# Kernel optimization log

Hardware: AMD Instinct MI355X
Metric: run time of the kernel (lower is better)

## Reference

```python
import jax, jax.numpy as jnp
import numpy as np

T = 2048           # tokens (single prefill sequence)
HIDDEN = 2048
H = 16             # num heads
D_NOPE = 128
D_ROPE = 64
D_V = 128
KV_LORA = 512
EPS = 1e-6
ROPE_THETA = 10000.0


def setup_inputs() -> dict:
    key = jax.random.key(0)
    ks = jax.random.split(key, 7)
    s = 0.02
    return {
        "positions": jnp.arange(T, dtype=jnp.int64) if jax.config.jax_enable_x64 else jnp.arange(T, dtype=jnp.int32),
        "hidden_states": jax.random.normal(ks[0], (T, HIDDEN), dtype=jnp.float32),
        "w_q": jax.random.normal(ks[1], (HIDDEN, H * (D_NOPE + D_ROPE)), dtype=jnp.float32) * s,
        "w_kv_a": jax.random.normal(ks[2], (HIDDEN, KV_LORA + D_ROPE), dtype=jnp.float32) * s,
        "kv_a_ln_w": jax.random.uniform(ks[3], (KV_LORA,), dtype=jnp.float32, minval=0.5, maxval=1.5),
        "w_kv_b": jax.random.normal(ks[4], (KV_LORA, H * (D_NOPE + D_V)), dtype=jnp.float32) * s,
        "w_o": jax.random.normal(ks[5], (H * D_V, HIDDEN), dtype=jnp.float32) * s,
    }


def _rms_norm(x, w):
    var = jnp.mean(jnp.square(x), axis=-1, keepdims=True)
    return x * jax.lax.rsqrt(var + EPS) * w


def _rope_nonneox(x, positions):
    # x: [..., D_ROPE], GPT-J (interleaved) style rotation
    inv_freq = 1.0 / (ROPE_THETA ** (jnp.arange(0, D_ROPE, 2, dtype=jnp.float32) / D_ROPE))
    freqs = positions.astype(jnp.float32)[:, None] * inv_freq  # [T, D_ROPE//2]
    cos, sin = jnp.cos(freqs), jnp.sin(freqs)
    # broadcast over head dim if present
    while cos.ndim < x.ndim:
        cos, sin = cos[:, None], sin[:, None]
    x1, x2 = x[..., 0::2], x[..., 1::2]
    o1 = x1 * cos - x2 * sin
    o2 = x2 * cos + x1 * sin
    return jnp.stack([o1, o2], axis=-1).reshape(x.shape)


def reference(positions, hidden_states, w_q, w_kv_a, kv_a_ln_w, w_kv_b, w_o):
    scaling = (D_NOPE + D_ROPE) ** -0.5
    # q projection (q_lora_rank is None branch)
    q = (hidden_states @ w_q).reshape(T, H, D_NOPE + D_ROPE)
    q_nope, q_pe = q[..., :D_NOPE], q[..., D_NOPE:]
    # compressed KV latent
    latent = hidden_states @ w_kv_a                 # [T, KV_LORA + D_ROPE]
    kv_a = _rms_norm(latent[:, :KV_LORA], kv_a_ln_w)
    k_pe = latent[:, KV_LORA:]                      # [T, D_ROPE], shared across heads
    # decompress to per-head k_nope and v (kv_b_proj)
    kv = (kv_a @ w_kv_b).reshape(T, H, D_NOPE + D_V)
    k_nope, v = kv[..., :D_NOPE], kv[..., D_NOPE:]
    # non-neox RoPE
    q_pe = _rope_nonneox(q_pe, positions)
    k_pe = _rope_nonneox(k_pe, positions)           # [T, D_ROPE]
    # concat rope parts (k_pe broadcast over heads)
    q_full = jnp.concatenate([q_nope, q_pe], axis=-1)                         # [T,H,192]
    k_full = jnp.concatenate([k_nope, jnp.broadcast_to(k_pe[:, None, :], (T, H, D_ROPE))], axis=-1)
    # causal MHA
    scores = jnp.einsum("qhd,khd->hqk", q_full, k_full) * scaling
    causal = positions[:, None] >= positions[None, :]
    scores = jnp.where(causal[None], scores, -jnp.inf)
    attn = jax.nn.softmax(scores, axis=-1)
    out = jnp.einsum("hqk,khd->qhd", attn, v).reshape(T, H * D_V)
    return out @ w_o
```

## Files before the change

### kernel.cpp

```cpp
#include <hip/hip_runtime.h>
#include <hip/hip_bf16.h>
#include <stdint.h>

#define T_SEQ   2048
#define NHEAD   16
#define NPAD1   3712

typedef short bf16x8  __attribute__((ext_vector_type(8)));
typedef float f32x4   __attribute__((ext_vector_type(4)));
typedef float f32x16  __attribute__((ext_vector_type(16)));

__device__ __forceinline__ unsigned short f2bf(float f) {
  union { float f; uint32_t u; } v; v.f = f;
  uint32_t u = v.u;
  uint32_t r = u + 0x7FFF + ((u >> 16) & 1);
  return (unsigned short)(r >> 16);
}

__device__ __forceinline__ void async16(const void* g, void* l) {
  __builtin_amdgcn_global_load_lds(
      (const __attribute__((address_space(1))) void*)g,
      (__attribute__((address_space(3))) void*)l, 16, 0, 0);
}

__device__ __forceinline__ void tr32(const float* __restrict__ in,
    unsigned short* __restrict__ out, int R, int C, int bx, int by,
    float (*tile)[33], int tid) {
  int r0 = bx * 32, c0 = by * 32;
  int tx = tid & 31, ty = tid >> 5;
  for (int i = 0; i < 4; i++)
    tile[ty + i * 8][tx] = in[(size_t)(r0 + ty + i * 8) * C + c0 + tx];
  __syncthreads();
  for (int i = 0; i < 4; i++) {
    int c = ty + i * 8;
    out[(size_t)(c0 + c) * R + r0 + tx] = f2bf(tile[tx][c]);
  }
}

__global__ __launch_bounds__(256) void prep_kernel(
    const float* __restrict__ hs, const float* __restrict__ w_q,
    const float* __restrict__ w_kv_a, const float* __restrict__ w_kv_b,
    const float* __restrict__ w_o,
    unsigned short* __restrict__ hs_bf, unsigned short* __restrict__ wcat_t,
    unsigned short* __restrict__ wkvb_t, unsigned short* __restrict__ wo_t) {
  __shared__ float tile[32][33];
  int bid = blockIdx.x, tid = threadIdx.x;
  if (bid < 4096) {
    int i = (bid * 256 + tid) * 4;
    float4 v = *(const float4*)(hs + i);
    ushort4 o; o.x = f2bf(v.x); o.y = f2bf(v.y); o.z = f2bf(v.z); o.w = f2bf(v.w);
    *(ushort4*)(hs_bf + i) = o;
  } else if (bid < 4096 + 6144) {
    int l = bid - 4096;
    tr32(w_q, wcat_t, 2048, 3072, l & 63, l >> 6, tile, tid);
  } else if (bid < 4096 + 6144 + 1152) {
    int l = bid - (4096 + 6144);
    tr32(w_kv_a, wcat_t + (size_t)3072 * 2048, 2048, 576, l & 63, l >> 6, tile, tid);
  } else if (bid < 4096 + 6144 + 1152 + 2048) {
    int l = bid - (4096 + 6144 + 1152);
    tr32(w_kv_b, wkvb_t, 512, 4096, l & 15, l >> 4, tile, tid);
  } else if (bid < 4096 + 6144 + 1152 + 2048 + 4096) {
    int l = bid - (4096 + 6144 + 1152 + 2048);
    tr32(w_o, wo_t, 2048, 2048, l & 63, l >> 6, tile, tid);
  } else {
    int l = bid - (4096 + 6144 + 1152 + 2048 + 4096);
    uint4 z = (uint4){0, 0, 0, 0};
    *(uint4*)(wcat_t + (size_t)3648 * 2048 + (size_t)(l * 256 + tid) * 8) = z;
  }
}

template<int TM, int OUT_BF16>
__global__ __launch_bounds__(256) void gemm_bt_kernel(
    const unsigned short* __restrict__ A, const unsigned short* __restrict__ B,
    void* __restrict__ Cv, int M, int N, int K) {
  constexpr int MT = TM / 32;
  __shared__ __align__(16) unsigned short Asm[2][TM * 32];
  __shared__ __align__(16) unsigned short Bsm[2][128 * 32];
  int tid = threadIdx.x, wid = tid >> 6, lane = tid & 63;
  int lrow = lane & 15, lquad = lane >> 4;
  int m0 = blockIdx.x * TM, n0 = blockIdx.y * 128;
  int wm = (wid & 1) * (TM / 2), wn = (wid >> 1) * 64;

  int row_s = tid >> 2, cc_s = tid & 3;
  const unsigned short* Ag0 = A + (size_t)(m0 + row_s) * K + cc_s * 8;
  const unsigned short* Ag1 = A + (size_t)(m0 + row_s + 64) * K + cc_s * 8;
  const unsigned short* Bg0 = B + (size_t)(n0 + row_s) * K + cc_s * 8;
  const unsigned short* Bg1 = B + (size_t)(n0 + row_s + 64) * K + cc_s * 8;

  f32x4 acc[MT][4];
  for (int i = 0; i < MT; i++) for (int j = 0; j < 4; j++) acc[i][j] = (f32x4){0.f,0.f,0.f,0.f};

  async16(Ag0, &Asm[0][tid * 8]);
  if (TM == 128) async16(Ag1, &Asm[0][2048 + tid * 8]);
  async16(Bg0, &Bsm[0][tid * 8]);
  async16(Bg1, &Bsm[0][2048 + tid * 8]);

  int cur = 0;
  for (int k0 = 0; k0 < K; k0 += 32) {
    __syncthreads();
    if (k0 + 32 < K) {
      int nxt = cur ^ 1, kk = k0 + 32;
      async16(Ag0 + kk, &Asm[nxt][tid * 8]);
      if (TM == 128) async16(Ag1 + kk, &Asm[nxt][2048 + tid * 8]);
      async16(Bg0 + kk, &Bsm[nxt][tid * 8]);
      async16(Bg1 + kk, &Bsm[nxt][2048 + tid * 8]);
    }
    const unsigned short* As = Asm[cur];
    const unsigned short* Bs = Bsm[cur];
    bf16x8 af[MT], bfr[4];
    for (int mt = 0; mt < MT; mt++)
      af[mt] = *(const bf16x8*)(As + (wm + mt * 16 + lrow) * 32 + lquad * 8);
    for (int nt = 0; nt < 4; nt++)
      bfr[nt] = *(const bf16x8*)(Bs + (wn + nt * 16 + lrow) * 32 + lquad * 8);
    for (int mt = 0; mt < MT; mt++)
      for (int nt = 0; nt < 4; nt++)
        acc[mt][nt] = __builtin_amdgcn_mfma_f32_16x16x32_bf16(af[mt], bfr[nt], acc[mt][nt], 0, 0, 0);
    cur ^= 1;
  }
  for (int mt = 0; mt < MT; mt++)
    for (int nt = 0; nt < 4; nt++) {
      int row = m0 + wm + mt * 16 + lquad * 4;
      int col = n0 + wn + nt * 16 + lrow;
      for (int r = 0; r < 4; r++) {
        if (OUT_BF16)
          ((unsigned short*)Cv)[(size_t)(row + r) * N + col] = f2bf(acc[mt][nt][r]);
        else
          ((float*)Cv)[(size_t)(row + r) * N + col] = acc[mt][nt][r];
      }
    }
}

__global__ __launch_bounds__(256) void postproc1_kernel(
    const float* __restrict__ q_lat,
    const float* __restrict__ ln_w,
    const int* __restrict__ positions,
    unsigned short* __restrict__ kv_a,
    unsigned short* __restrict__ q_full,
    unsigned short* __restrict__ k_pe)
{
  int t = blockIdx.x, tid = threadIdx.x;
  const float* row = q_lat + (size_t)t * NPAD1;
  const float scaling = 0.07216878364870323f;

  float v0 = row[3072 + tid], v1 = row[3072 + 256 + tid];
  float ss = v0 * v0 + v1 * v1;
  for (int m = 1; m < 64; m <<= 1) ss += __shfl_xor(ss, m, 64);
  __shared__ float red[4];
  if ((tid & 63) == 0) red[tid >> 6] = ss;
  __shared__ float kro[64], cf[32], sf[32];
  float pos = (float)positions[t];
  if (tid < 32) {
    float inv_freq = powf(10000.f, -(float)(2 * tid) / 64.f);
    float c, s; sincosf(pos * inv_freq, &s, &c);
    cf[tid] = c; sf[tid] = s;
    float x1 = row[3584 + 2 * tid], x2 = row[3584 + 2 * tid + 1];
    kro[2 * tid]     = x1 * c - x2 * s;
    kro[2 * tid + 1] = x2 * c + x1 * s;
  }
  __syncthreads();
  float rstd = rsqrtf((red[0] + red[1] + red[2] + red[3]) * (1.f / 512.f) + 1e-6f);
  kv_a[(size_t)t * 512 + tid]       = f2bf(v0 * rstd * ln_w[tid]);
  kv_a[(size_t)t * 512 + 256 + tid] = f2bf(v1 * rstd * ln_w[256 + tid]);
  if (tid < 64) k_pe[(size_t)t * 64 + tid] = f2bf(kro[tid]);

  for (int i = tid; i < NHEAD * 128; i += 256) {
    int h = i >> 7, d = i & 127;
    q_full[((size_t)h * T_SEQ + t) * 192 + d] = f2bf(row[h * 192 + d] * scaling);
  }
  for (int i = tid; i < NHEAD * 32; i += 256) {
    int h = i >> 5, p = i & 31;
    float c = cf[p], s = sf[p];
    float x1 = row[h * 192 + 128 + 2 * p], x2 = row[h * 192 + 128 + 2 * p + 1];
    q_full[((size_t)h * T_SEQ + t) * 192 + 128 + 2 * p]     = f2bf((x1 * c - x2 * s) * scaling);
    q_full[((size_t)h * T_SEQ + t) * 192 + 128 + 2 * p + 1] = f2bf((x2 * c + x1 * s) * scaling);
  }
}

__global__ __launch_bounds__(256) void kvpost_kernel(
    const unsigned short* __restrict__ kv_b,
    const unsigned short* __restrict__ k_pe,
    unsigned short* __restrict__ k_full,
    unsigned short* __restrict__ v_t) {
  __shared__ unsigned short tile[32][41];
  int bid = blockIdx.x, tid = threadIdx.x;
  if (bid < 3072) {
    int idx = bid * 256 + tid;
    int cc = idx % 24, rest = idx / 24;
    int t = rest & (T_SEQ - 1), h = rest >> 11;
    uint4 v = (cc < 16)
        ? *(const uint4*)(kv_b + (size_t)t * 4096 + h * 256 + cc * 8)
        : *(const uint4*)(k_pe + (size_t)t * 64 + (cc - 16) * 8);
    *(uint4*)(k_full + (size_t)idx * 8) = v;
  } else {
    int l = bid - 3072;
    int h = l >> 8, t0 = (l & 63) * 32, d0 = ((l >> 6) & 3) * 32;
    int tx = tid & 31, ty = tid >> 5;
    for (int i = 0; i < 4; i++)
      tile[ty + i * 8][tx] = kv_b[(size_t)(t0 + ty + i * 8) * 4096 + h * 256 + 128 + d0 + tx];
    __syncthreads();
    for (int i = 0; i < 4; i++)
      v_t[((size_t)h * 128 + d0 + ty + i * 8) * T_SEQ + t0 + tx] = tile[tx][ty + i * 8];
  }
}

#define PP 76
__global__ __launch_bounds__(256, 2) void flash_kernel(
    const unsigned short* __restrict__ q_full,
    const unsigned short* __restrict__ k_full,
    const unsigned short* __restrict__ v_t,
    unsigned short* __restrict__ attn_out)
{
  __shared__ __align__(16) unsigned short Ksm[2][1536 * 8];
  __shared__ __align__(16) unsigned short Vsm[1024 * 8];
  __shared__ __align__(16) unsigned short Psm[64 * PP];
  __shared__ float Lred[2][64];
  int h = blockIdx.x;
  int y = blockIdx.y;
  int qb = (y < 16) ? (31 - y) : (y - 16);
  int tid = threadIdx.x, wid = tid >> 6, lane = tid & 63;
  int l31 = lane & 31, l5 = lane >> 5, x7 = l31 & 7;
  int rq = wid & 1, kq = wid >> 1;

  const unsigned short* kh = k_full + (size_t)h * T_SEQ * 192;
  const unsigned short* vh = v_t    + (size_t)h * 128 * T_SEQ;

  int gK[6], gV[4];
  #pragma unroll
  for (int j = 0; j < 6; j++) {
    int s = tid + j * 256, row = s / 24, cm = s - row * 24;
    gK[j] = row * 192 + (cm ^ (row & 7)) * 8;
  }
  #pragma unroll
  for (int j = 0; j < 4; j++) {
    int s = tid + j * 256, d = s >> 3;
    gV[j] = d * T_SEQ + ((s & 7) ^ (d & 7)) * 8;
  }
  int kxo[12];
  #pragma unroll
  for (int kc = 0; kc < 12; kc++)
    kxo[kc] = (kq * 32 + l31) * 192 + ((kc * 2 + l5) ^ x7) * 8;
  int vxb[2];
  #pragma unroll
  for (int ntv = 0; ntv < 2; ntv++) vxb[ntv] = (kq * 64 + ntv * 32 + l31) * 64;

  bf16x8 qf[12];
  {
    const unsigned short* qrow =
        q_full + ((size_t)h * T_SEQ + qb * 64 + rq * 32 + l31) * 192 + l5 * 8;
    #pragma unroll
    for (int kc = 0; kc < 12; kc++) qf[kc] = *(const bf16x8*)(qrow + kc * 16);
  }
  f32x16 oacc[2];
  for (int i = 0; i < 2; i++) oacc[i] = (f32x16)(0.f);
  float lsum[16];
  #pragma unroll
  for (int r = 0; r < 16; r++) lsum[r] = 0.f;
  int rl[16];
  #pragma unroll
  for (int r = 0; r < 16; r++) rl[r] = (r & 3) + 8 * (r >> 2) + 4 * l5;

  #pragma unroll
  for (int j = 0; j < 6; j++) async16(kh + gK[j], &Ksm[0][(tid + j * 256) * 8]);

  int cur = 0;
  for (int kb = 0; kb <= qb; kb++) {
    __syncthreads();
    {
      const unsigned short* vb = vh + kb * 64;
      #pragma unroll
      for (int j = 0; j < 4; j++) async16(vb + gV[j], &Vsm[(tid + j * 256) * 8]);
    }
    const unsigned short* Ks = Ksm[cur];
    f32x16 sacc = (f32x16)(0.f);
    #pragma unroll
    for (int kc = 0; kc < 12; kc++) {
      bf16x8 kf = *(const bf16x8*)(Ks + kxo[kc]);
      sacc = __builtin_amdgcn_mfma_f32_32x32x16_bf16(qf[kc], kf, sacc, 0, 0, 0);
    }
    if (kb == qb) {
      int col_g = kb * 64 + kq * 32 + l31;
      int row_b = qb * 64 + rq * 32;
      #pragma unroll
      for (int r = 0; r < 16; r++)
        if (col_g > row_b + rl[r]) sacc[r] = -1e30f;
    }
    #pragma unroll
    for (int r = 0; r < 16; r++) {
      float p = __expf(sacc[r]);
      sacc[r] = p;
      lsum[r] += p;
    }
    #pragma unroll
    for (int r = 0; r < 16; r++)
      Psm[(rq * 32 + rl[r]) * PP + kq * 32 + l31] = f2bf(sacc[r]);
    __syncthreads();
    if (kb < qb) {
      const unsigned short* kb1 = kh + (size_t)(kb + 1) * 64 * 192;
      #pragma unroll
      for (int j = 0; j < 6; j++) async16(kb1 + gK[j], &Ksm[cur ^ 1][(tid + j * 256) * 8]);
    }
    #pragma unroll
    for (int kc = 0; kc < 4; kc++) {
      bf16x8 pf = *(const bf16x8*)(Psm + (rq * 32 + l31) * PP + kc * 16 + l5 * 8);
      #pragma unroll
      for (int ntv = 0; ntv < 2; ntv++) {
        bf16x8 vf = *(const bf16x8*)(Vsm + vxb[ntv] + ((kc * 2 + l5) ^ x7) * 8);
        oacc[ntv] = __builtin_amdgcn_mfma_f32_32x32x16_bf16(pf, vf, oacc[ntv], 0, 0, 0);
      }
    }
    cur ^= 1;
  }

  #pragma unroll
  for (int r = 0; r < 16; r++) {
    float s = lsum[r];
    s += __shfl_xor(s, 1, 64);
    s += __shfl_xor(s, 2, 64);
    s += __shfl_xor(s, 4, 64);
    s += __shfl_xor(s, 8, 64);
    s += __shfl_xor(s, 16, 64);
    lsum[r] = s;
  }
  if (l31 == 0)
    #pragma unroll
    for (int r = 0; r < 16; r++) Lred[kq][rq * 32 + rl[r]] = lsum[r];
  __syncthreads();
  #pragma unroll
  for (int r = 0; r < 16; r++) {
    int row_l = rq * 32 + rl[r];
    float inv = 1.f / (Lred[0][row_l] + Lred[1][row_l]);
    int row_g = qb * 64 + row_l;
    #pragma unroll
    for (int ntv = 0; ntv < 2; ntv++)
      attn_out[(size_t)row_g * 2048 + h * 128 + kq * 64 + ntv * 32 + l31] =
          f2bf(oacc[ntv][r] * inv);
  }
}

extern "C" void kernel_launch(void* const* d_in, const int* in_sizes, int n_in,
                              void* d_out, int out_size, void* d_ws, size_t ws_size,
                              hipStream_t stream) {
  const int*   positions = (const int*)d_in[0];
  const float* hs     = (const float*)d_in[1];
  const float* w_q    = (const float*)d_in[2];
  const float* w_kv_a = (const float*)d_in[3];
  const float* ln_w   = (const float*)d_in[4];
  const float* w_kv_b = (const float*)d_in[5];
  const float* w_o    = (const float*)d_in[6];
  float* out = (float*)d_out;

  char* ws = (char*)d_ws;
  size_t off = 0;
  auto alloc = [&](size_t bytes) { void* p = ws + off; off += (bytes + 255) & ~(size_t)255; return p; };
  unsigned short* hs_bf   = (unsigned short*)alloc((size_t)2048 * 2048 * 2);
  unsigned short* wcat_t  = (unsigned short*)alloc((size_t)NPAD1 * 2048 * 2);
  float*          q_lat   = (float*)alloc((size_t)2048 * NPAD1 * 4);
  unsigned short* kv_a_bf = (unsigned short*)alloc((size_t)2048 * 512 * 2);
  unsigned short* wkvb_t  = (unsigned short*)alloc((size_t)4096 * 512 * 2);
  unsigned short* kv_b    = (unsigned short*)alloc((size_t)2048 * 4096 * 2);
  unsigned short* q_full  = (unsigned short*)alloc((size_t)NHEAD * 2048 * 192 * 2);
  unsigned short* k_pe    = (unsigned short*)alloc((size_t)2048 * 64 * 2);
  unsigned short* k_full  = (unsigned short*)alloc((size_t)NHEAD * 2048 * 192 * 2);
  unsigned short* v_t     = (unsigned short*)alloc((size_t)NHEAD * 128 * 2048 * 2);
  unsigned short* attn_o  = (unsigned short*)alloc((size_t)2048 * 2048 * 2);
  unsigned short* wo_t    = (unsigned short*)alloc((size_t)2048 * 2048 * 2);

  prep_kernel<<<17600, 256, 0, stream>>>(hs, w_q, w_kv_a, w_kv_b, w_o,
                                         hs_bf, wcat_t, wkvb_t, wo_t);
  gemm_bt_kernel<128, 0><<<dim3(16, 29), 256, 0, stream>>>(hs_bf, wcat_t, q_lat, 2048, NPAD1, 2048);
  postproc1_kernel<<<2048, 256, 0, stream>>>(q_lat, ln_w, positions, kv_a_bf, q_full, k_pe);
  gemm_bt_kernel<128, 1><<<dim3(16, 32), 256, 0, stream>>>(kv_a_bf, wkvb_t, kv_b, 2048, 4096, 512);
  kvpost_kernel<<<7168, 256, 0, stream>>>(kv_b, k_pe, k_full, v_t);
  flash_kernel<<<dim3(16, 32), 256, 0, stream>>>(q_full, k_full, v_t, attn_o);
  gemm_bt_kernel<64, 0><<<dim3(32, 16), 256, 0, stream>>>(attn_o, wo_t, out, 2048, 2048, 2048);
}
```

Before: 280.6 us.

## Fuse head-layout scatter into GEMM epilogues, deepen K tile, enlarge transpose tiles

```diff
diff --git a/kernel.cpp b/kernel.cpp
--- a/kernel.cpp
+++ b/kernel.cpp
@@ -5,6 +5,7 @@
 #define T_SEQ   2048
 #define NHEAD   16
 #define NPAD1   3712
+#define QSCALE  0.07216878364870323f
 
 typedef short bf16x8  __attribute__((ext_vector_type(8)));
 typedef float f32x4   __attribute__((ext_vector_type(4)));
@@ -23,16 +24,16 @@
       (__attribute__((address_space(3))) void*)l, 16, 0, 0);
 }
 
-__device__ __forceinline__ void tr32(const float* __restrict__ in,
+__device__ __forceinline__ void tr64(const float* __restrict__ in,
     unsigned short* __restrict__ out, int R, int C, int bx, int by,
-    float (*tile)[33], int tid) {
-  int r0 = bx * 32, c0 = by * 32;
-  int tx = tid & 31, ty = tid >> 5;
-  for (int i = 0; i < 4; i++)
-    tile[ty + i * 8][tx] = in[(size_t)(r0 + ty + i * 8) * C + c0 + tx];
+    float (*tile)[65], int tid) {
+  int r0 = bx * 64, c0 = by * 64;
+  int tx = tid & 63, ty = tid >> 6;
+  for (int i = 0; i < 16; i++)
+    tile[ty + i * 4][tx] = in[(size_t)(r0 + ty + i * 4) * C + c0 + tx];
   __syncthreads();
-  for (int i = 0; i < 4; i++) {
-    int c = ty + i * 8;
+  for (int i = 0; i < 16; i++) {
+    int c = ty + i * 4;
     out[(size_t)(c0 + c) * R + r0 + tx] = f2bf(tile[tx][c]);
   }
 }
@@ -43,95 +44,128 @@
     const float* __restrict__ w_o,
     unsigned short* __restrict__ hs_bf, unsigned short* __restrict__ wcat_t,
     unsigned short* __restrict__ wkvb_t, unsigned short* __restrict__ wo_t) {
-  __shared__ float tile[32][33];
+  __shared__ float tile[64][65];
   int bid = blockIdx.x, tid = threadIdx.x;
   if (bid < 4096) {
     int i = (bid * 256 + tid) * 4;
     float4 v = *(const float4*)(hs + i);
     ushort4 o; o.x = f2bf(v.x); o.y = f2bf(v.y); o.z = f2bf(v.z); o.w = f2bf(v.w);
     *(ushort4*)(hs_bf + i) = o;
-  } else if (bid < 4096 + 6144) {
+  } else if (bid < 4096 + 1536) {
     int l = bid - 4096;
-    tr32(w_q, wcat_t, 2048, 3072, l & 63, l >> 6, tile, tid);
-  } else if (bid < 4096 + 6144 + 1152) {
-    int l = bid - (4096 + 6144);
-    tr32(w_kv_a, wcat_t + (size_t)3072 * 2048, 2048, 576, l & 63, l >> 6, tile, tid);
-  } else if (bid < 4096 + 6144 + 1152 + 2048) {
-    int l = bid - (4096 + 6144 + 1152);
-    tr32(w_kv_b, wkvb_t, 512, 4096, l & 15, l >> 4, tile, tid);
-  } else if (bid < 4096 + 6144 + 1152 + 2048 + 4096) {
-    int l = bid - (4096 + 6144 + 1152 + 2048);
-    tr32(w_o, wo_t, 2048, 2048, l & 63, l >> 6, tile, tid);
+    tr64(w_q, wcat_t, 2048, 3072, l & 31, l >> 5, tile, tid);
+  } else if (bid < 4096 + 1536 + 288) {
+    int l = bid - (4096 + 1536);
+    tr64(w_kv_a, wcat_t + (size_t)3072 * 2048, 2048, 576, l % 32, l / 32, tile, tid);
+  } else if (bid < 4096 + 1536 + 288 + 512) {
+    int l = bid - (4096 + 1536 + 288);
+    tr64(w_kv_b, wkvb_t, 512, 4096, l & 7, l >> 3, tile, tid);
+  } else if (bid < 4096 + 1536 + 288 + 512 + 1024) {
+    int l = bid - (4096 + 1536 + 288 + 512);
+    tr64(w_o, wo_t, 2048, 2048, l & 31, l >> 5, tile, tid);
   } else {
-    int l = bid - (4096 + 6144 + 1152 + 2048 + 4096);
+    int l = bid - (4096 + 1536 + 288 + 512 + 1024);
     uint4 z = (uint4){0, 0, 0, 0};
     *(uint4*)(wcat_t + (size_t)3648 * 2048 + (size_t)(l * 256 + tid) * 8) = z;
   }
 }
 
-template<int TM, int OUT_BF16>
+template<int TM, int MODE>
 __global__ __launch_bounds__(256) void gemm_bt_kernel(
     const unsigned short* __restrict__ A, const unsigned short* __restrict__ B,
-    void* __restrict__ Cv, int M, int N, int K) {
+    void* __restrict__ Cv, void* __restrict__ aux0, void* __restrict__ aux1,
+    int M, int N, int K) {
   constexpr int MT = TM / 32;
-  __shared__ __align__(16) unsigned short Asm[2][TM * 32];
-  __shared__ __align__(16) unsigned short Bsm[2][128 * 32];
+  __shared__ __align__(16) unsigned short Asm[2][TM * 64];
+  __shared__ __align__(16) unsigned short Bsm[2][128 * 64];
   int tid = threadIdx.x, wid = tid >> 6, lane = tid & 63;
   int lrow = lane & 15, lquad = lane >> 4;
   int m0 = blockIdx.x * TM, n0 = blockIdx.y * 128;
   int wm = (wid & 1) * (TM / 2), wn = (wid >> 1) * 64;
 
   int row_s = tid >> 2, cc_s = tid & 3;
-  const unsigned short* Ag0 = A + (size_t)(m0 + row_s) * K + cc_s * 8;
-  const unsigned short* Ag1 = A + (size_t)(m0 + row_s + 64) * K + cc_s * 8;
-  const unsigned short* Bg0 = B + (size_t)(n0 + row_s) * K + cc_s * 8;
-  const unsigned short* Bg1 = B + (size_t)(n0 + row_s + 64) * K + cc_s * 8;
+  const unsigned short* Ag = A + (size_t)(m0 + row_s) * K + cc_s * 8;
+  const unsigned short* Bg = B + (size_t)(n0 + row_s) * K + cc_s * 8;
+  const size_t rowK64 = (size_t)64 * K;
 
   f32x4 acc[MT][4];
   for (int i = 0; i < MT; i++) for (int j = 0; j < 4; j++) acc[i][j] = (f32x4){0.f,0.f,0.f,0.f};
 
-  async16(Ag0, &Asm[0][tid * 8]);
-  if (TM == 128) async16(Ag1, &Asm[0][2048 + tid * 8]);
-  async16(Bg0, &Bsm[0][tid * 8]);
-  async16(Bg1, &Bsm[0][2048 + tid * 8]);
+  auto stage = [&](int kk, int buf) {
+    async16(Ag + kk,      &Asm[buf][tid * 8]);
+    async16(Ag + kk + 32, &Asm[buf][(256 + tid) * 8]);
+    if (TM == 128) {
+      async16(Ag + kk + rowK64,      &Asm[buf][(512 + tid) * 8]);
+      async16(Ag + kk + rowK64 + 32, &Asm[buf][(768 + tid) * 8]);
+    }
+    async16(Bg + kk,      &Bsm[buf][tid * 8]);
+    async16(Bg + kk + 32, &Bsm[buf][(256 + tid) * 8]);
+    async16(Bg + kk + rowK64,      &Bsm[buf][(512 + tid) * 8]);
+    async16(Bg + kk + rowK64 + 32, &Bsm[buf][(768 + tid) * 8]);
+  };
+
+  stage(0, 0);
+  int abase = (wm >> 6) * 4096 + ((wm & 63) + lrow) * 32 + lquad * 8;
+  int bbase = (wn >> 6) * 4096 + lrow * 32 + lquad * 8;
 
   int cur = 0;
-  for (int k0 = 0; k0 < K; k0 += 32) {
+  for (int k0 = 0; k0 < K; k0 += 64) {
     __syncthreads();
-    if (k0 + 32 < K) {
-      int nxt = cur ^ 1, kk = k0 + 32;
-      async16(Ag0 + kk, &Asm[nxt][tid * 8]);
-      if (TM == 128) async16(Ag1 + kk, &Asm[nxt][2048 + tid * 8]);
-      async16(Bg0 + kk, &Bsm[nxt][tid * 8]);
-      async16(Bg1 + kk, &Bsm[nxt][2048 + tid * 8]);
-    }
+    if (k0 + 64 < K) stage(k0 + 64, cur ^ 1);
     const unsigned short* As = Asm[cur];
     const unsigned short* Bs = Bsm[cur];
-    bf16x8 af[MT], bfr[4];
-    for (int mt = 0; mt < MT; mt++)
-      af[mt] = *(const bf16x8*)(As + (wm + mt * 16 + lrow) * 32 + lquad * 8);
-    for (int nt = 0; nt < 4; nt++)
-      bfr[nt] = *(const bf16x8*)(Bs + (wn + nt * 16 + lrow) * 32 + lquad * 8);
-    for (int mt = 0; mt < MT; mt++)
+    #pragma unroll
+    for (int step = 0; step < 2; step++) {
+      bf16x8 af[MT], bfr[4];
+      #pragma unroll
+      for (int mt = 0; mt < MT; mt++)
+        af[mt] = *(const bf16x8*)(As + abase + step * 2048 + mt * 512);
+      #pragma unroll
       for (int nt = 0; nt < 4; nt++)
-        acc[mt][nt] = __builtin_amdgcn_mfma_f32_16x16x32_bf16(af[mt], bfr[nt], acc[mt][nt], 0, 0, 0);
+        bfr[nt] = *(const bf16x8*)(Bs + bbase + step * 2048 + nt * 512);
+      #pragma unroll
+      for (int mt = 0; mt < MT; mt++)
+        #pragma unroll
+        for (int nt = 0; nt < 4; nt++)
+          acc[mt][nt] = __builtin_amdgcn_mfma_f32_16x16x32_bf16(af[mt], bfr[nt], acc[mt][nt], 0, 0, 0);
+    }
     cur ^= 1;
   }
+
   for (int mt = 0; mt < MT; mt++)
     for (int nt = 0; nt < 4; nt++) {
       int row = m0 + wm + mt * 16 + lquad * 4;
       int col = n0 + wn + nt * 16 + lrow;
       for (int r = 0; r < 4; r++) {
-        if (OUT_BF16)
-          ((unsigned short*)Cv)[(size_t)(row + r) * N + col] = f2bf(acc[mt][nt][r]);
-        else
-          ((float*)Cv)[(size_t)(row + r) * N + col] = acc[mt][nt][r];
+        float v = acc[mt][nt][r];
+        if (MODE == 0) {
+          ((float*)Cv)[(size_t)(row + r) * N + col] = v;
+        } else if (MODE == 1) {
+          ((unsigned short*)Cv)[(size_t)(row + r) * N + col] = f2bf(v);
+        } else if (MODE == 2) {
+          if (n0 < 3072) {
+            int h = (unsigned)col / 192u, d = col - h * 192;
+            if (d < 128)
+              ((unsigned short*)Cv)[((size_t)h * T_SEQ + row + r) * 192 + d] = f2bf(v * QSCALE);
+            else
+              ((float*)aux0)[(size_t)(row + r) * 1024 + h * 64 + (d - 128)] = v * QSCALE;
+          } else {
+            ((float*)aux1)[(size_t)(row + r) * 640 + (col - 3072)] = v;
+          }
+        } else {
+          int h = col >> 8, c = col & 255;
+          if (c < 128)
+            ((unsigned short*)Cv)[((size_t)h * T_SEQ + row + r) * 192 + c] = f2bf(v);
+          else
+            ((unsigned short*)aux0)[(size_t)(row + r) * 2048 + h * 128 + (c - 128)] = f2bf(v);
+        }
       }
     }
 }
 
 __global__ __launch_bounds__(256) void postproc1_kernel(
-    const float* __restrict__ q_lat,
+    const float* __restrict__ lat,
+    const float* __restrict__ qpe,
     const float* __restrict__ ln_w,
     const int* __restrict__ positions,
     unsigned short* __restrict__ kv_a,
@@ -139,10 +173,9 @@
     unsigned short* __restrict__ k_pe)
 {
   int t = blockIdx.x, tid = threadIdx.x;
-  const float* row = q_lat + (size_t)t * NPAD1;
-  const float scaling = 0.07216878364870323f;
-
-  float v0 = row[3072 + tid], v1 = row[3072 + 256 + tid];
+  const float* row = lat + (size_t)t * 640;
+
+  float v0 = row[tid], v1 = row[256 + tid];
   float ss = v0 * v0 + v1 * v1;
   for (int m = 1; m < 64; m <<= 1) ss += __shfl_xor(ss, m, 64);
   __shared__ float red[4];
@@ -153,7 +186,7 @@
     float inv_freq = powf(10000.f, -(float)(2 * tid) / 64.f);
     float c, s; sincosf(pos * inv_freq, &s, &c);
     cf[tid] = c; sf[tid] = s;
-    float x1 = row[3584 + 2 * tid], x2 = row[3584 + 2 * tid + 1];
+    float x1 = row[512 + 2 * tid], x2 = row[512 + 2 * tid + 1];
     kro[2 * tid]     = x1 * c - x2 * s;
     kro[2 * tid + 1] = x2 * c + x1 * s;
   }
@@ -163,40 +196,36 @@
   kv_a[(size_t)t * 512 + 256 + tid] = f2bf(v1 * rstd * ln_w[256 + tid]);
   if (tid < 64) k_pe[(size_t)t * 64 + tid] = f2bf(kro[tid]);
 
-  for (int i = tid; i < NHEAD * 128; i += 256) {
-    int h = i >> 7, d = i & 127;
-    q_full[((size_t)h * T_SEQ + t) * 192 + d] = f2bf(row[h * 192 + d] * scaling);
-  }
-  for (int i = tid; i < NHEAD * 32; i += 256) {
+  #pragma unroll
+  for (int ii = 0; ii < 2; ii++) {
+    int i = tid + ii * 256;
     int h = i >> 5, p = i & 31;
     float c = cf[p], s = sf[p];
-    float x1 = row[h * 192 + 128 + 2 * p], x2 = row[h * 192 + 128 + 2 * p + 1];
-    q_full[((size_t)h * T_SEQ + t) * 192 + 128 + 2 * p]     = f2bf((x1 * c - x2 * s) * scaling);
-    q_full[((size_t)h * T_SEQ + t) * 192 + 128 + 2 * p + 1] = f2bf((x2 * c + x1 * s) * scaling);
+    float x1 = qpe[(size_t)t * 1024 + h * 64 + 2 * p];
+    float x2 = qpe[(size_t)t * 1024 + h * 64 + 2 * p + 1];
+    q_full[((size_t)h * T_SEQ + t) * 192 + 128 + 2 * p]     = f2bf(x1 * c - x2 * s);
+    q_full[((size_t)h * T_SEQ + t) * 192 + 128 + 2 * p + 1] = f2bf(x2 * c + x1 * s);
   }
 }
 
 __global__ __launch_bounds__(256) void kvpost_kernel(
-    const unsigned short* __restrict__ kv_b,
     const unsigned short* __restrict__ k_pe,
+    const unsigned short* __restrict__ v_n,
     unsigned short* __restrict__ k_full,
     unsigned short* __restrict__ v_t) {
   __shared__ unsigned short tile[32][41];
   int bid = blockIdx.x, tid = threadIdx.x;
-  if (bid < 3072) {
+  if (bid < 1024) {
     int idx = bid * 256 + tid;
-    int cc = idx % 24, rest = idx / 24;
-    int t = rest & (T_SEQ - 1), h = rest >> 11;
-    uint4 v = (cc < 16)
-        ? *(const uint4*)(kv_b + (size_t)t * 4096 + h * 256 + cc * 8)
-        : *(const uint4*)(k_pe + (size_t)t * 64 + (cc - 16) * 8);
-    *(uint4*)(k_full + (size_t)idx * 8) = v;
+    int cc = idx & 7, t = (idx >> 3) & (T_SEQ - 1), h = idx >> 14;
+    uint4 v = *(const uint4*)(k_pe + (size_t)t * 64 + cc * 8);
+    *(uint4*)(k_full + ((size_t)h * T_SEQ + t) * 192 + 128 + cc * 8) = v;
   } else {
-    int l = bid - 3072;
+    int l = bid - 1024;
     int h = l >> 8, t0 = (l & 63) * 32, d0 = ((l >> 6) & 3) * 32;
     int tx = tid & 31, ty = tid >> 5;
     for (int i = 0; i < 4; i++)
-      tile[ty + i * 8][tx] = kv_b[(size_t)(t0 + ty + i * 8) * 4096 + h * 256 + 128 + d0 + tx];
+      tile[ty + i * 8][tx] = v_n[(size_t)(t0 + ty + i * 8) * 2048 + h * 128 + d0 + tx];
     __syncthreads();
     for (int i = 0; i < 4; i++)
       v_t[((size_t)h * 128 + d0 + ty + i * 8) * T_SEQ + t0 + tx] = tile[tx][ty + i * 8];
@@ -354,23 +383,27 @@
   auto alloc = [&](size_t bytes) { void* p = ws + off; off += (bytes + 255) & ~(size_t)255; return p; };
   unsigned short* hs_bf   = (unsigned short*)alloc((size_t)2048 * 2048 * 2);
   unsigned short* wcat_t  = (unsigned short*)alloc((size_t)NPAD1 * 2048 * 2);
-  float*          q_lat   = (float*)alloc((size_t)2048 * NPAD1 * 4);
+  float*          lat     = (float*)alloc((size_t)2048 * 640 * 4);
+  float*          qpe     = (float*)alloc((size_t)2048 * 1024 * 4);
   unsigned short* kv_a_bf = (unsigned short*)alloc((size_t)2048 * 512 * 2);
   unsigned short* wkvb_t  = (unsigned short*)alloc((size_t)4096 * 512 * 2);
-  unsigned short* kv_b    = (unsigned short*)alloc((size_t)2048 * 4096 * 2);
   unsigned short* q_full  = (unsigned short*)alloc((size_t)NHEAD * 2048 * 192 * 2);
   unsigned short* k_pe    = (unsigned short*)alloc((size_t)2048 * 64 * 2);
   unsigned short* k_full  = (unsigned short*)alloc((size_t)NHEAD * 2048 * 192 * 2);
+  unsigned short* v_n     = (unsigned short*)alloc((size_t)2048 * 2048 * 2);
   unsigned short* v_t     = (unsigned short*)alloc((size_t)NHEAD * 128 * 2048 * 2);
   unsigned short* attn_o  = (unsigned short*)alloc((size_t)2048 * 2048 * 2);
   unsigned short* wo_t    = (unsigned short*)alloc((size_t)2048 * 2048 * 2);
 
-  prep_kernel<<<17600, 256, 0, stream>>>(hs, w_q, w_kv_a, w_kv_b, w_o,
-                                         hs_bf, wcat_t, wkvb_t, wo_t);
-  gemm_bt_kernel<128, 0><<<dim3(16, 29), 256, 0, stream>>>(hs_bf, wcat_t, q_lat, 2048, NPAD1, 2048);
-  postproc1_kernel<<<2048, 256, 0, stream>>>(q_lat, ln_w, positions, kv_a_bf, q_full, k_pe);
-  gemm_bt_kernel<128, 1><<<dim3(16, 32), 256, 0, stream>>>(kv_a_bf, wkvb_t, kv_b, 2048, 4096, 512);
-  kvpost_kernel<<<7168, 256, 0, stream>>>(kv_b, k_pe, k_full, v_t);
+  prep_kernel<<<7520, 256, 0, stream>>>(hs, w_q, w_kv_a, w_kv_b, w_o,
+                                        hs_bf, wcat_t, wkvb_t, wo_t);
+  gemm_bt_kernel<128, 2><<<dim3(16, 29), 256, 0, stream>>>(
+      hs_bf, wcat_t, q_full, qpe, lat, 2048, NPAD1, 2048);
+  postproc1_kernel<<<2048, 256, 0, stream>>>(lat, qpe, ln_w, positions, kv_a_bf, q_full, k_pe);
+  gemm_bt_kernel<128, 3><<<dim3(16, 32), 256, 0, stream>>>(
+      kv_a_bf, wkvb_t, k_full, v_n, nullptr, 2048, 4096, 512);
+  kvpost_kernel<<<5120, 256, 0, stream>>>(k_pe, v_n, k_full, v_t);
   flash_kernel<<<dim3(16, 32), 256, 0, stream>>>(q_full, k_full, v_t, attn_o);
-  gemm_bt_kernel<64, 0><<<dim3(32, 16), 256, 0, stream>>>(attn_o, wo_t, out, 2048, 2048, 2048);
-}
+  gemm_bt_kernel<64, 0><<<dim3(32, 16), 256, 0, stream>>>(
+      attn_o, wo_t, out, nullptr, nullptr, 2048, 2048, 2048);
+}
```

Result: slower. 395.9 us (+41.1%).
